# Kernel tuning notes

Measured on AMD Instinct MI355X. Metric: run time of the kernel, lower is better.

Reference implementation:

```python
import jax, jax.numpy as jnp
import numpy as np

N_HEAD = 16


def setup_inputs() -> dict:
    key = jax.random.key(0)
    k1, k2, k3 = jax.random.split(key, 3)
    B, T, C = 2, 2048, 1024
    x = jax.random.normal(k1, (B, T, C), dtype=jnp.float32)
    Wqkv = jax.random.normal(k2, (C, 3 * C), dtype=jnp.float32) * 0.02
    bqkv = jnp.zeros((3 * C,), dtype=jnp.float32)
    Wproj = jax.random.normal(k3, (C, C), dtype=jnp.float32) * 0.02
    bproj = jnp.zeros((C,), dtype=jnp.float32)
    return {"x": x, "Wqkv": Wqkv, "bqkv": bqkv, "Wproj": Wproj, "bproj": bproj}


def reference(x, Wqkv, bqkv, Wproj, bproj):
    b, t, c = x.shape
    h = N_HEAD
    d = c // h  # head_dim
    # qkv projection, split into q,k,v per head: (b,t,3,h,d)
    qkv = (x @ Wqkv + bqkv).reshape(b, t, 3, h, d)
    q, k, v = qkv[:, :, 0], qkv[:, :, 1], qkv[:, :, 2]  # each (b,t,h,d)
    # Faithful quirk of original: n_state = head_dim // heads, scale = 1/sqrt(n_state)
    scale = jnp.float32(1.0 / np.sqrt(d // h))
    # attn_mode == 'all': dense non-causal attention
    w = jnp.einsum('bqhd,bkhd->bhqk', q, k)  # (b,h,t,t)
    w = jax.nn.softmax(w * scale, axis=-1)
    a = jnp.einsum('bhqk,bkhd->bqhd', w, v).reshape(b, t, c)
    return a @ Wproj + bproj
```

## Files before the change

kernel.cpp:

```cpp
#include <hip/hip_runtime.h>

typedef float floatx4 __attribute__((ext_vector_type(4)));
typedef float floatx16 __attribute__((ext_vector_type(16)));
typedef __bf16 bf16x8 __attribute__((ext_vector_type(8)));
typedef __bf16 bf16x4 __attribute__((ext_vector_type(4)));
typedef __bf16 bf16x2 __attribute__((ext_vector_type(2)));
typedef float floatx2 __attribute__((ext_vector_type(2)));

#define MFMA16 __builtin_amdgcn_mfma_f32_16x16x32_bf16
#define MFMA32 __builtin_amdgcn_mfma_f32_32x32x16_bf16

typedef const __attribute__((address_space(1))) void* gas_t;
typedef __attribute__((address_space(3))) void* las_t;
#define GLD16(g, l) __builtin_amdgcn_global_load_lds((gas_t)(g), (las_t)(l), 16, 0, 0)

static __device__ __forceinline__ unsigned short f2bf(float f) {
  union { float f; unsigned int u; } v; v.f = f;
  unsigned int r = v.u + 0x7fffu + ((v.u >> 16) & 1u);
  return (unsigned short)(r >> 16);
}

static __device__ __forceinline__ unsigned pk2(float a, float b) {
  floatx2 v; v[0] = a; v[1] = b;
  union { bf16x2 h; unsigned u; } u;
  u.h = __builtin_convertvector(v, bf16x2);
  return u.u;
}

static __device__ __forceinline__ void cast_transpose_tile(
    const float* __restrict__ in, unsigned short* __restrict__ out,
    int R, int C, int bx, int by) {
  const int r0 = by * 64, c0 = bx * 64;
  const int tid = threadIdx.x;
  __shared__ float tl[64][65];
  const int rr = tid >> 4, cc = (tid & 15) * 4;
#pragma unroll
  for (int i = 0; i < 4; ++i) {
    int row = rr + i * 16;
    float4 v = *(const float4*)(in + (size_t)(r0 + row) * C + c0 + cc);
    tl[row][cc] = v.x; tl[row][cc + 1] = v.y;
    tl[row][cc + 2] = v.z; tl[row][cc + 3] = v.w;
  }
  __syncthreads();
  const int cl = tid >> 2, rbase = (tid & 3) * 16;
  unsigned short o[16];
#pragma unroll
  for (int j = 0; j < 16; ++j) o[j] = f2bf(tl[rbase + j][cl]);
  unsigned short* dst = out + (size_t)(c0 + cl) * R + r0 + rbase;
  *(uint4*)dst = *(uint4*)o;
  *(uint4*)(dst + 8) = *(uint4*)(o + 8);
}

__global__ __launch_bounds__(256) void prologue_kernel(
    const float* __restrict__ x, unsigned short* __restrict__ Xb,
    const float* __restrict__ Wqkv, unsigned short* __restrict__ Wqkvt,
    const float* __restrict__ Wproj, unsigned short* __restrict__ Wprojt) {
  const int bid = blockIdx.x;
  if (bid < 4096) {
    int i = bid * 256 + threadIdx.x;
    float4 v = ((const float4*)x)[i];
    ushort4 o;
    o.x = f2bf(v.x); o.y = f2bf(v.y); o.z = f2bf(v.z); o.w = f2bf(v.w);
    ((ushort4*)Xb)[i] = o;
  } else if (bid < 4096 + 768) {
    int b2 = bid - 4096;
    cast_transpose_tile(Wqkv, Wqkvt, 1024, 3072, b2 % 48, b2 / 48);
  } else {
    int b3 = bid - 4096 - 768;
    cast_transpose_tile(Wproj, Wprojt, 1024, 1024, b3 % 16, b3 / 16);
  }
}

__global__ __launch_bounds__(256) void gemm_qkv(
    const unsigned short* __restrict__ A,
    const unsigned short* __restrict__ Bt,
    const float* __restrict__ bias,
    unsigned short* __restrict__ Q,
    unsigned short* __restrict__ Kc,
    unsigned short* __restrict__ Vt) {
  const int K = 1024;
  const int m0 = blockIdx.y * 128, n0 = blockIdx.x * 128;
  const int tid = threadIdx.x, w = tid >> 6, l = tid & 63;
  const int l16 = l & 15, lq = l >> 4;
  const int wm = w >> 1, wn = w & 1;
  const int which = n0 >> 10;

  __shared__ __align__(16) unsigned short SH[32768];

  floatx4 acc[4][4] = {};

  int sA[4], sB[4];
  unsigned ldso[4];
#pragma unroll
  for (int j = 0; j < 4; ++j) {
    int s = j * 256 + tid;
    int row = s >> 3, blk = (s & 7) ^ (row & 7);
    sA[j] = (m0 + row) * K + blk * 8;
    sB[j] = (n0 + row) * K + blk * 8;
    ldso[j] = (unsigned)(j * 256 + w * 64) * 8;
  }

#pragma unroll
  for (int j = 0; j < 4; ++j) {
    GLD16(A + sA[j], SH + ldso[j]);
    GLD16(Bt + sB[j], SH + 8192 + ldso[j]);
  }

  if (which == 2) {
    for (int k0 = 0; k0 < K; k0 += 64) {
      __syncthreads();
      const int cur = (k0 >> 6) & 1;
      if (k0 + 64 < K) {
        const int nxt = cur ^ 1;
#pragma unroll
        for (int j = 0; j < 4; ++j) {
          GLD16(A + sA[j] + k0 + 64, SH + nxt * 16384 + ldso[j]);
          GLD16(Bt + sB[j] + k0 + 64, SH + nxt * 16384 + 8192 + ldso[j]);
        }
      }
      const unsigned short* As = SH + cur * 16384;
      const unsigned short* Bs = SH + cur * 16384 + 8192;
#pragma unroll
      for (int kk = 0; kk < 2; ++kk) {
        bf16x8 af[4], bf[4];
#pragma unroll
        for (int mi = 0; mi < 4; ++mi) {
          int row = wm * 64 + mi * 16 + l16;
          int blk = (kk * 4 + lq) ^ (l16 & 7);
          af[mi] = *(const bf16x8*)(As + row * 64 + blk * 8);
        }
#pragma unroll
        for (int ni = 0; ni < 4; ++ni) {
          int row = wn * 64 + ni * 16 + l16;
          int blk = (kk * 4 + lq) ^ (l16 & 7);
          bf[ni] = *(const bf16x8*)(Bs + row * 64 + blk * 8);
        }
#pragma unroll
        for (int ni = 0; ni < 4; ++ni)
#pragma unroll
          for (int mi = 0; mi < 4; ++mi)
            acc[mi][ni] = MFMA16(af[mi], bf[ni], acc[mi][ni], 0, 0, 0);
      }
    }
    float bv[4];
#pragma unroll
    for (int ni = 0; ni < 4; ++ni) bv[ni] = bias[n0 + wn * 64 + ni * 16 + l16];
    __syncthreads();
    unsigned short* E = SH + w * 2304;
    const int bh = (m0 >> 11) * 16 + ((n0 & 1023) >> 6) + wn;
    const int tt0 = (m0 & 2047) + wm * 64;
    const int m8 = l & 7, bc = 16 * (m8 >> 1) + 4 * (m8 & 1);
#pragma unroll
    for (int p = 0; p < 2; ++p) {
#pragma unroll
      for (int n2 = 0; n2 < 2; ++n2) {
        int ni = p * 2 + n2;
#pragma unroll
        for (int mi = 0; mi < 4; ++mi) {
          floatx4 vv = acc[mi][ni] + bv[ni];
          *(bf16x4*)(E + (n2 * 16 + l16) * 72 + mi * 16 + lq * 4) =
              __builtin_convertvector(vv, bf16x4);
        }
      }
#pragma unroll
      for (int s = 0; s < 4; ++s) {
        int dl = s * 8 + (l >> 3);
        union { bf16x4 h[2]; bf16x8 v; } uu;
        uu.h[0] = *(const bf16x4*)(E + dl * 72 + bc);
        uu.h[1] = *(const bf16x4*)(E + dl * 72 + bc + 8);
        *(bf16x8*)(Vt + ((size_t)bh * 64 + p * 32 + dl) * 2048 + tt0 +
                   m8 * 8) = uu.v;
      }
    }
  } else {
    for (int k0 = 0; k0 < K; k0 += 64) {
      __syncthreads();
      const int cur = (k0 >> 6) & 1;
      if (k0 + 64 < K) {
        const int nxt = cur ^ 1;
#pragma unroll
        for (int j = 0; j < 4; ++j) {
          GLD16(A + sA[j] + k0 + 64, SH + nxt * 16384 + ldso[j]);
          GLD16(Bt + sB[j] + k0 + 64, SH + nxt * 16384 + 8192 + ldso[j]);
        }
      }
      const unsigned short* As = SH + cur * 16384;
      const unsigned short* Bs = SH + cur * 16384 + 8192;
#pragma unroll
      for (int kk = 0; kk < 2; ++kk) {
        bf16x8 af[4], bf[4];
#pragma unroll
        for (int mi = 0; mi < 4; ++mi) {
          int row = wm * 64 + mi * 16 + l16;
          int blk = (kk * 4 + lq) ^ (l16 & 7);
          af[mi] = *(const bf16x8*)(As + row * 64 + blk * 8);
        }
#pragma unroll
        for (int ni = 0; ni < 4; ++ni) {
          int row = wn * 64 + ni * 16 + l16;
          int blk = (kk * 4 + lq) ^ (l16 & 7);
          bf[ni] = *(const bf16x8*)(Bs + row * 64 + blk * 8);
        }
#pragma unroll
        for (int ni = 0; ni < 4; ++ni)
#pragma unroll
          for (int mi = 0; mi < 4; ++mi)
            acc[mi][ni] = MFMA16(bf[ni], af[mi], acc[mi][ni], 0, 0, 0);
      }
    }
    const float sc = (which == 0) ? 0.7213475204444817f : 1.0f;
    unsigned short* dst = (which == 0) ? Q : Kc;
    __syncthreads();
    unsigned short* E = SH + w * 2304;
    const int bh = (m0 >> 11) * 16 + ((n0 & 1023) >> 6) + wn;
    const size_t gbase = ((size_t)bh * 2048 + (m0 & 2047) + wm * 64) * 64;
#pragma unroll
    for (int p = 0; p < 2; ++p) {
#pragma unroll
      for (int m2 = 0; m2 < 2; ++m2) {
        int mi = p * 2 + m2;
#pragma unroll
        for (int ni = 0; ni < 4; ++ni) {
          int col0 = n0 + wn * 64 + ni * 16 + lq * 4;
          floatx4 bv = *(const floatx4*)(bias + col0);
          floatx4 vv = (acc[mi][ni] + bv) * sc;
          *(bf16x4*)(E + (m2 * 16 + l16) * 72 + ni * 16 + lq * 4) =
              __builtin_convertvector(vv, bf16x4);
        }
      }
#pragma unroll
      for (int s = 0; s < 4; ++s) {
        int rl = s * 8 + (l >> 3);
        bf16x8 vv = *(const bf16x8*)(E + rl * 72 + (l & 7) * 8);
        *(bf16x8*)(dst + gbase + (size_t)(p * 32 + rl) * 64 + (l & 7) * 8) =
            vv;
      }
    }
  }
}

__global__ __launch_bounds__(256, 2) void attn_kernel(
    const unsigned short* __restrict__ Q,
    const unsigned short* __restrict__ Kc,
    const unsigned short* __restrict__ Vt,
    unsigned short* __restrict__ AO) {
  const int T = 2048;
  const int bid = blockIdx.x;
  const int lin = (bid & 7) * 64 + (bid >> 3);
  const int bh = lin >> 4, q0 = (lin & 15) * 128;
  const int tid = threadIdx.x, w = tid >> 6, l = tid & 63;
  const int r31 = l & 31, g = l >> 5;
  const int kh = w >> 1, wq = w & 1;
  const int h128 = tid & 127;

  __shared__ __align__(16) unsigned short KVs[2][2][2][4096];

  bf16x8 qf[2][4];
#pragma unroll
  for (int qt = 0; qt < 2; ++qt) {
    const unsigned short* qr =
        Q + ((size_t)bh * T + q0 + wq * 64 + qt * 32 + r31) * 64 + g * 8;
#pragma unroll
    for (int ds = 0; ds < 4; ++ds) qf[qt][ds] = *(const bf16x8*)(qr + ds * 16);
  }

  floatx16 o_acc[2][2] = {};
  float l_lane[2] = {0.f, 0.f};

  const unsigned short* kbase = Kc + (size_t)bh * T * 64;
  const unsigned short* vbase = Vt + (size_t)bh * 64 * T;
  int kro[4], vro[4];
  unsigned ldso[4];
#pragma unroll
  for (int j = 0; j < 4; ++j) {
    int s = j * 128 + h128;
    int row = s >> 3, blk = (s & 7) ^ (row & 7);
    kro[j] = row * 64 + blk * 8;
    vro[j] = row * T + blk * 8;
    ldso[j] = (unsigned)(j * 128 + (h128 & 64)) * 8;
  }

  {
    const int c0 = kh * 16;
#pragma unroll
    for (int j = 0; j < 4; ++j) {
      GLD16(kbase + c0 * 4096 + kro[j], &KVs[0][kh][0][ldso[j]]);
      GLD16(vbase + c0 * 64 + vro[j], &KVs[1][kh][0][ldso[j]]);
    }
  }

  for (int it = 0; it < 16; ++it) {
    __syncthreads();
    if (it + 1 < 16) {
      const int cn = kh * 16 + it + 1, nb = (it + 1) & 1;
#pragma unroll
      for (int j = 0; j < 4; ++j) {
        GLD16(kbase + cn * 4096 + kro[j], &KVs[0][kh][nb][ldso[j]]);
        GLD16(vbase + cn * 64 + vro[j], &KVs[1][kh][nb][ldso[j]]);
      }
    }
    const unsigned short* kb = &KVs[0][kh][it & 1][0];
    const unsigned short* vb = &KVs[1][kh][it & 1][0];

    bf16x8 kf[2][4];
#pragma unroll
    for (int kt = 0; kt < 2; ++kt) {
      const int row = kt * 32 + r31, rx = row & 7;
      const unsigned short* kr = kb + row * 64;
#pragma unroll
      for (int ds = 0; ds < 4; ++ds)
        kf[kt][ds] = *(const bf16x8*)(kr + ((ds * 2 + g) ^ rx) * 8);
    }

    bf16x8 pf[2][4];
#pragma unroll
    for (int qt = 0; qt < 2; ++qt) {
#pragma unroll
      for (int kt = 0; kt < 2; ++kt) {
        floatx16 z = {};
#pragma unroll
        for (int ds = 0; ds < 4; ++ds)
          z = MFMA32(kf[kt][ds], qf[qt][ds], z, 0, 0, 0);

        float pe[16];
#pragma unroll
        for (int r = 0; r < 16; ++r) pe[r] = __builtin_amdgcn_exp2f(z[r]);
        l_lane[qt] += (((pe[0] + pe[1]) + (pe[2] + pe[3])) +
                       ((pe[4] + pe[5]) + (pe[6] + pe[7]))) +
                      (((pe[8] + pe[9]) + (pe[10] + pe[11])) +
                       ((pe[12] + pe[13]) + (pe[14] + pe[15])));
#pragma unroll
        for (int s2 = 0; s2 < 2; ++s2) {
          union { unsigned u[4]; bf16x8 v; } pu;
          pu.u[0] = pk2(pe[8 * s2 + 0], pe[8 * s2 + 1]);
          pu.u[1] = pk2(pe[8 * s2 + 2], pe[8 * s2 + 3]);
          pu.u[2] = pk2(pe[8 * s2 + 4], pe[8 * s2 + 5]);
          pu.u[3] = pk2(pe[8 * s2 + 6], pe[8 * s2 + 7]);
          pf[qt][kt * 2 + s2] = pu.v;
        }
      }
    }

#pragma unroll
    for (int dt = 0; dt < 2; ++dt) {
      const int row = dt * 32 + r31, rx = row & 7;
      const unsigned short* vr = vb + row * 64;
#pragma unroll
      for (int s = 0; s < 4; ++s) {
        bf16x8 vf = *(const bf16x8*)(vr + ((s * 2 + g) ^ rx) * 8);
#pragma unroll
        for (int qt = 0; qt < 2; ++qt)
          o_acc[qt][dt] = MFMA32(vf, pf[qt][s], o_acc[qt][dt], 0, 0, 0);
      }
    }
  }

  __syncthreads();
  float* oex = (float*)&KVs[0][0][0][0];
  float* Lex = oex + 128 * 68;
  if (kh == 1) {
    float* r = oex + (wq * 64 + l) * 68;
#pragma unroll
    for (int qt = 0; qt < 2; ++qt) {
#pragma unroll
      for (int dt = 0; dt < 2; ++dt)
#pragma unroll
        for (int rq = 0; rq < 4; ++rq) {
          floatx4 ov;
          ov[0] = o_acc[qt][dt][rq * 4 + 0];
          ov[1] = o_acc[qt][dt][rq * 4 + 1];
          ov[2] = o_acc[qt][dt][rq * 4 + 2];
          ov[3] = o_acc[qt][dt][rq * 4 + 3];
          *(floatx4*)(r + qt * 32 + dt * 16 + rq * 4) = ov;
        }
      Lex[(wq * 64 + l) * 2 + qt] = l_lane[qt];
    }
  }
  __syncthreads();
  if (kh == 0) {
    const float* r = oex + (wq * 64 + l) * 68;
    const int b = bh >> 4, h = bh & 15;
#pragma unroll
    for (int qt = 0; qt < 2; ++qt) {
      float ls = l_lane[qt] + Lex[(wq * 64 + l) * 2 + qt];
      ls += __shfl_xor(ls, 32, 64);
      float inv = 1.0f / ls;
      const int t = q0 + wq * 64 + qt * 32 + r31;
      unsigned short* ao = AO + ((size_t)b * 2048 + t) * 1024 + h * 64;
#pragma unroll
      for (int dt = 0; dt < 2; ++dt)
#pragma unroll
        for (int rq = 0; rq < 4; ++rq) {
          floatx4 ov;
          ov[0] = o_acc[qt][dt][rq * 4 + 0];
          ov[1] = o_acc[qt][dt][rq * 4 + 1];
          ov[2] = o_acc[qt][dt][rq * 4 + 2];
          ov[3] = o_acc[qt][dt][rq * 4 + 3];
          ov += *(const floatx4*)(r + qt * 32 + dt * 16 + rq * 4);
          ov *= inv;
          *(bf16x4*)(ao + dt * 32 + rq * 8 + g * 4) =
              __builtin_convertvector(ov, bf16x4);
        }
    }
  }
}

__global__ __launch_bounds__(256) void gemm_proj(
    const unsigned short* __restrict__ A,
    const unsigned short* __restrict__ Bt,
    const float* __restrict__ bias,
    float* __restrict__ out) {
  const int K = 1024, N = 1024;
  const int m0 = blockIdx.y * 128, n0 = blockIdx.x * 64;
  const int tid = threadIdx.x, w = tid >> 6, l = tid & 63;
  const int l16 = l & 15, lq = l >> 4;

  __shared__ __align__(16) unsigned short SH[24576];

  floatx4 acc[2][4] = {};

  int sA[4], sB[2];
  unsigned ldsoA[4], ldsoB[2];
#pragma unroll
  for (int j = 0; j < 4; ++j) {
    int s = j * 256 + tid;
    int row = s >> 3, blk = (s & 7) ^ (row & 7);
    sA[j] = (m0 + row) * K + blk * 8;
    ldsoA[j] = (unsigned)(j * 256 + w * 64) * 8;
  }
#pragma unroll
  for (int j = 0; j < 2; ++j) {
    int s = j * 256 + tid;
    int row = s >> 3, blk = (s & 7) ^ (row & 7);
    sB[j] = (n0 + row) * K + blk * 8;
    ldsoB[j] = (unsigned)(j * 256 + w * 64) * 8;
  }

#pragma unroll
  for (int j = 0; j < 4; ++j) GLD16(A + sA[j], SH + ldsoA[j]);
#pragma unroll
  for (int j = 0; j < 2; ++j) GLD16(Bt + sB[j], SH + 8192 + ldsoB[j]);

  for (int k0 = 0; k0 < K; k0 += 64) {
    __syncthreads();
    const int cur = (k0 >> 6) & 1;
    if (k0 + 64 < K) {
      const int nxt = cur ^ 1;
#pragma unroll
      for (int j = 0; j < 4; ++j)
        GLD16(A + sA[j] + k0 + 64, SH + nxt * 12288 + ldsoA[j]);
#pragma unroll
      for (int j = 0; j < 2; ++j)
        GLD16(Bt + sB[j] + k0 + 64, SH + nxt * 12288 + 8192 + ldsoB[j]);
    }
    const unsigned short* As = SH + cur * 12288;
    const unsigned short* Bs = SH + cur * 12288 + 8192;
#pragma unroll
    for (int kk = 0; kk < 2; ++kk) {
      bf16x8 af[2], bf[4];
#pragma unroll
      for (int mi = 0; mi < 2; ++mi) {
        int row = w * 32 + mi * 16 + l16;
        int blk = (kk * 4 + lq) ^ (l16 & 7);
        af[mi] = *(const bf16x8*)(As + row * 64 + blk * 8);
      }
#pragma unroll
      for (int ni = 0; ni < 4; ++ni) {
        int row = ni * 16 + l16;
        int blk = (kk * 4 + lq) ^ (l16 & 7);
        bf[ni] = *(const bf16x8*)(Bs + row * 64 + blk * 8);
      }
#pragma unroll
      for (int ni = 0; ni < 4; ++ni)
#pragma unroll
        for (int mi = 0; mi < 2; ++mi)
          acc[mi][ni] = MFMA16(bf[ni], af[mi], acc[mi][ni], 0, 0, 0);
    }
  }

#pragma unroll
  for (int mi = 0; mi < 2; ++mi) {
    int t = m0 + w * 32 + mi * 16 + l16;
#pragma unroll
    for (int ni = 0; ni < 4; ++ni) {
      int col0 = n0 + ni * 16 + lq * 4;
      floatx4 bv = *(const floatx4*)(bias + col0);
      *(floatx4*)(out + (size_t)t * N + col0) = acc[mi][ni] + bv;
    }
  }
}

extern "C" void kernel_launch(void* const* d_in, const int* in_sizes, int n_in,
                              void* d_out, int out_size, void* d_ws,
                              size_t ws_size, hipStream_t stream) {
  const float* x     = (const float*)d_in[0];
  const float* Wqkv  = (const float*)d_in[1];
  const float* bqkv  = (const float*)d_in[2];
  const float* Wproj = (const float*)d_in[3];
  const float* bproj = (const float*)d_in[4];
  float* out = (float*)d_out;

  unsigned short* Xb     = (unsigned short*)d_ws;
  unsigned short* Wqkvt  = Xb + 4194304;
  unsigned short* Wprojt = Wqkvt + 3145728;
  unsigned short* Qb     = Wprojt + 1048576;
  unsigned short* Kb     = Qb + 4194304;
  unsigned short* Vtb    = Kb + 4194304;
  unsigned short* AOb    = Vtb + 4194304;

  prologue_kernel<<<5120, 256, 0, stream>>>(x, Xb, Wqkv, Wqkvt, Wproj, Wprojt);
  gemm_qkv<<<dim3(24, 32), 256, 0, stream>>>(Xb, Wqkvt, bqkv, Qb, Kb, Vtb);
  attn_kernel<<<512, 256, 0, stream>>>(Qb, Kb, Vtb, AOb);
  gemm_proj<<<dim3(16, 32), 256, 0, stream>>>(AOb, Wprojt, bproj, out);
}
```

Measured before the change: 169.8 us.

## Load K/V fragments directly from global memory instead of LDS staging

Removes the double-buffered LDS staging of K and V tiles (global_load_lds with swizzle) and the per-iteration block barrier. Each wave now loads its K and V MFMA fragments straight from global memory into registers. The intent is to drop the barrier and LDS round-trip costs. In exchange, waves sharing a key half no longer share one LDS copy, so global/L2 traffic for K/V doubles, and there is no explicit prefetch to hide load latency.

```diff
diff --git a/kernel.cpp b/kernel.cpp
--- a/kernel.cpp
+++ b/kernel.cpp
@@ -251,9 +251,9 @@
   const int tid = threadIdx.x, w = tid >> 6, l = tid & 63;
   const int r31 = l & 31, g = l >> 5;
   const int kh = w >> 1, wq = w & 1;
-  const int h128 = tid & 127;
-
-  __shared__ __align__(16) unsigned short KVs[2][2][2][4096];
+
+  __shared__ __align__(16) float oex[128 * 68];
+  __shared__ float Lex[256];
 
   bf16x8 qf[2][4];
 #pragma unroll
@@ -267,50 +267,27 @@
   floatx16 o_acc[2][2] = {};
   float l_lane[2] = {0.f, 0.f};
 
-  const unsigned short* kbase = Kc + (size_t)bh * T * 64;
-  const unsigned short* vbase = Vt + (size_t)bh * 64 * T;
-  int kro[4], vro[4];
-  unsigned ldso[4];
-#pragma unroll
-  for (int j = 0; j < 4; ++j) {
-    int s = j * 128 + h128;
-    int row = s >> 3, blk = (s & 7) ^ (row & 7);
-    kro[j] = row * 64 + blk * 8;
-    vro[j] = row * T + blk * 8;
-    ldso[j] = (unsigned)(j * 128 + (h128 & 64)) * 8;
-  }
-
-  {
-    const int c0 = kh * 16;
-#pragma unroll
-    for (int j = 0; j < 4; ++j) {
-      GLD16(kbase + c0 * 4096 + kro[j], &KVs[0][kh][0][ldso[j]]);
-      GLD16(vbase + c0 * 64 + vro[j], &KVs[1][kh][0][ldso[j]]);
-    }
-  }
-
-  for (int it = 0; it < 16; ++it) {
-    __syncthreads();
-    if (it + 1 < 16) {
-      const int cn = kh * 16 + it + 1, nb = (it + 1) & 1;
-#pragma unroll
-      for (int j = 0; j < 4; ++j) {
-        GLD16(kbase + cn * 4096 + kro[j], &KVs[0][kh][nb][ldso[j]]);
-        GLD16(vbase + cn * 64 + vro[j], &KVs[1][kh][nb][ldso[j]]);
-      }
-    }
-    const unsigned short* kb = &KVs[0][kh][it & 1][0];
-    const unsigned short* vb = &KVs[1][kh][it & 1][0];
-
+  const unsigned short* kbase =
+      Kc + ((size_t)bh * T + kh * 1024) * 64 + (size_t)r31 * 64 + g * 8;
+  const unsigned short* vbase =
+      Vt + ((size_t)bh * 64 + r31) * T + kh * 1024 + g * 8;
+
+  for (int c = 0; c < 16; ++c) {
+    const unsigned short* kc = kbase + c * 64 * 64;
     bf16x8 kf[2][4];
 #pragma unroll
-    for (int kt = 0; kt < 2; ++kt) {
-      const int row = kt * 32 + r31, rx = row & 7;
-      const unsigned short* kr = kb + row * 64;
+    for (int kt = 0; kt < 2; ++kt)
 #pragma unroll
       for (int ds = 0; ds < 4; ++ds)
-        kf[kt][ds] = *(const bf16x8*)(kr + ((ds * 2 + g) ^ rx) * 8);
-    }
+        kf[kt][ds] = *(const bf16x8*)(kc + kt * 32 * 64 + ds * 16);
+
+    const unsigned short* vc = vbase + c * 64;
+    bf16x8 vf[2][4];
+#pragma unroll
+    for (int dt = 0; dt < 2; ++dt)
+#pragma unroll
+      for (int s = 0; s < 4; ++s)
+        vf[dt][s] = *(const bf16x8*)(vc + (size_t)dt * 32 * T + s * 16);
 
     bf16x8 pf[2][4];
 #pragma unroll
@@ -342,22 +319,15 @@
     }
 
 #pragma unroll
-    for (int dt = 0; dt < 2; ++dt) {
-      const int row = dt * 32 + r31, rx = row & 7;
-      const unsigned short* vr = vb + row * 64;
-#pragma unroll
-      for (int s = 0; s < 4; ++s) {
-        bf16x8 vf = *(const bf16x8*)(vr + ((s * 2 + g) ^ rx) * 8);
+    for (int dt = 0; dt < 2; ++dt)
+#pragma unroll
+      for (int s = 0; s < 4; ++s)
 #pragma unroll
         for (int qt = 0; qt < 2; ++qt)
-          o_acc[qt][dt] = MFMA32(vf, pf[qt][s], o_acc[qt][dt], 0, 0, 0);
-      }
-    }
+          o_acc[qt][dt] = MFMA32(vf[dt][s], pf[qt][s], o_acc[qt][dt], 0, 0, 0);
   }
 
   __syncthreads();
-  float* oex = (float*)&KVs[0][0][0][0];
-  float* Lex = oex + 128 * 68;
   if (kh == 1) {
     float* r = oex + (wq * 64 + l) * 68;
 #pragma unroll
```

Result: slower. 191.8 us (+13.0%).
